# Kernel tuning notes

Measured on AMD Instinct MI355X. Metric: run time of the kernel, lower is better.

Reference implementation:

```python
import jax, jax.numpy as jnp
import numpy as np

TEMPERATURE = 0.1
N, D = 4096, 1024


def setup_inputs() -> dict:
    key = jax.random.key(0)
    k1, k2 = jax.random.split(key)
    return {
        "embeddings1": jax.random.normal(k1, (N, D), dtype=jnp.float32),
        "embeddings2": jax.random.normal(k2, (N, D), dtype=jnp.float32),
    }


def reference(embeddings1, embeddings2):
    # L2-normalize rows (eps matches torch F.normalize default 1e-12)
    e1 = embeddings1 / jnp.maximum(jnp.linalg.norm(embeddings1, axis=1, keepdims=True), 1e-12)
    e2 = embeddings2 / jnp.maximum(jnp.linalg.norm(embeddings2, axis=1, keepdims=True), 1e-12)

    # [N, N] pairwise logits; one GEMM replaces the N^2 Python-loop dots
    logits = jnp.einsum("nd,md->nm", e1, e2) / TEMPERATURE
    expS = jnp.exp(logits)
    diag = jnp.diagonal(expS)

    # denominators EXCLUDE the diagonal term (as in the original loop slicing)
    row_denom = jnp.sum(expS, axis=1) - diag  # sum over j != i of exp(s_ij)
    col_denom = jnp.sum(expS, axis=0) - diag  # sum over i != j of exp(s_ij)

    log_diag = jnp.diagonal(logits)
    sim_12 = jnp.sum(log_diag - jnp.log(row_denom))
    sim_21 = jnp.sum(log_diag - jnp.log(col_denom))
    return (-sim_12, -sim_21)
```

## Files before the change

### kernel.cpp

```cpp
#include <hip/hip_runtime.h>
#include <hip/hip_bf16.h>
#include <stdint.h>

#define NN 4096
#define DD 1024
#define INV_T 10.0f

typedef float f32x4 __attribute__((ext_vector_type(4)));
typedef __bf16 bf16x8 __attribute__((ext_vector_type(8)));

__device__ __forceinline__ unsigned short f2bf(float x) {
  return __builtin_bit_cast(unsigned short, __float2bfloat16(x));
}

__device__ __forceinline__ void gload_lds16(const void* g, void* l) {
  __builtin_amdgcn_global_load_lds(
      (const __attribute__((address_space(1))) void*)g,
      (__attribute__((address_space(3))) void*)l, 16, 0, 0);
}

__global__ __launch_bounds__(256) void nrm_kernel(
    const float* __restrict__ e1, const float* __restrict__ e2,
    unsigned short* __restrict__ e1n, unsigned short* __restrict__ e2n,
    float* __restrict__ log_diag, float* __restrict__ exp_diag,
    float* __restrict__ row_sum, float* __restrict__ col_sum)
{
  const int row  = blockIdx.x;
  const int tid  = threadIdx.x;
  const int lane = tid & 63;
  const int wave = tid >> 6;
  const int64_t base = (int64_t)row * DD;

  const float4 v1 = *reinterpret_cast<const float4*>(e1 + base + tid * 4);
  const float4 v2 = *reinterpret_cast<const float4*>(e2 + base + tid * 4);

  float ss1 = v1.x*v1.x + v1.y*v1.y + v1.z*v1.z + v1.w*v1.w;
  float ss2 = v2.x*v2.x + v2.y*v2.y + v2.z*v2.z + v2.w*v2.w;
  float d12 = v1.x*v2.x + v1.y*v2.y + v1.z*v2.z + v1.w*v2.w;

  #pragma unroll
  for (int off = 1; off < 64; off <<= 1) {
    ss1 += __shfl_xor(ss1, off);
    ss2 += __shfl_xor(ss2, off);
    d12 += __shfl_xor(d12, off);
  }

  __shared__ float red[3][4];
  if (lane == 0) { red[0][wave] = ss1; red[1][wave] = ss2; red[2][wave] = d12; }
  __syncthreads();
  ss1 = red[0][0] + red[0][1] + red[0][2] + red[0][3];
  ss2 = red[1][0] + red[1][1] + red[1][2] + red[1][3];
  d12 = red[2][0] + red[2][1] + red[2][2] + red[2][3];

  const float inv1 = 1.0f / fmaxf(sqrtf(ss1), 1e-12f);
  const float inv2 = 1.0f / fmaxf(sqrtf(ss2), 1e-12f);

  if (tid == 0) {
    const float ld = d12 * inv1 * inv2 * INV_T;
    log_diag[row] = ld;
    exp_diag[row] = __expf(ld);
    row_sum[row] = 0.0f;
    col_sum[row] = 0.0f;
  }

  ushort4 o1, o2;
  o1.x = f2bf(v1.x * inv1); o1.y = f2bf(v1.y * inv1);
  o1.z = f2bf(v1.z * inv1); o1.w = f2bf(v1.w * inv1);
  o2.x = f2bf(v2.x * inv2); o2.y = f2bf(v2.y * inv2);
  o2.z = f2bf(v2.z * inv2); o2.w = f2bf(v2.w * inv2);
  *reinterpret_cast<ushort4*>(e1n + base + tid * 4) = o1;
  *reinterpret_cast<ushort4*>(e2n + base + tid * 4) = o2;
}

__device__ __forceinline__ void stage_khalf(
    const unsigned short* __restrict__ src, int row_base, int kcol,
    unsigned short (*dst)[32], int wave, int lane)
{
  const int r0 = wave * 16 + (lane >> 2);
  const int c  = ((lane & 3) ^ ((lane >> 3) & 3)) * 8;
  gload_lds16(src + (int64_t)(row_base + r0) * DD + kcol + c,
              &dst[wave * 16][0]);
  gload_lds16(src + (int64_t)(row_base + 128 + r0) * DD + kcol + c,
              &dst[128 + wave * 16][0]);
}

__global__ __launch_bounds__(512, 2) void gemm_kernel(
    const unsigned short* __restrict__ A,
    const unsigned short* __restrict__ B,
    float* __restrict__ row_sum, float* __restrict__ col_sum)
{
  __shared__ __align__(16) unsigned short lds_a[2][2][256][32];
  __shared__ __align__(16) unsigned short lds_b[2][2][256][32];

  const int tid  = threadIdx.x;
  const int lane = tid & 63;
  const int wave = tid >> 6;
  const int wm = wave >> 2;
  const int wn = wave & 3;

  const int bid = blockIdx.x;
  const int xcd = bid & 7;
  const int k   = bid >> 3;
  const int brow = ((xcd >> 1) * 4 + (k >> 3)) * 256;
  const int bcol = ((xcd & 1) * 8 + (k & 7)) * 256;

  const int fr = lane & 15;
  const int fq = lane >> 4;
  const int rslot = (fq ^ ((fr >> 1) & 3)) * 8;

  f32x4 acc[8][4] = {};

  stage_khalf(A, brow, 0,  lds_a[0][0], wave, lane);
  stage_khalf(B, bcol, 0,  lds_b[0][0], wave, lane);
  stage_khalf(A, brow, 32, lds_a[0][1], wave, lane);
  stage_khalf(B, bcol, 32, lds_b[0][1], wave, lane);

#define PHASE(KK)                                                               \
  {                                                                             \
    if (pf) { stage_khalf(A, brow, kn + (KK)*32, lds_a[n][KK], wave, lane);     \
              stage_khalf(B, bcol, kn + (KK)*32, lds_b[n][KK], wave, lane); }   \
    bf16x8 a0[4], a1[4], bv[4];                                                 \
    _Pragma("unroll")                                                           \
    for (int i = 0; i < 4; ++i)                                                 \
      a0[i] = *reinterpret_cast<const bf16x8*>(                                 \
          &lds_a[c][KK][wm*128 + i*16 + fr][rslot]);                            \
    _Pragma("unroll")                                                           \
    for (int i = 0; i < 4; ++i)                                                 \
      bv[i] = *reinterpret_cast<const bf16x8*>(                                 \
          &lds_b[c][KK][wn*64 + i*16 + fr][rslot]);                             \
    _Pragma("unroll")                                                           \
    for (int i = 0; i < 4; ++i)                                                 \
      a1[i] = *reinterpret_cast<const bf16x8*>(                                 \
          &lds_a[c][KK][wm*128 + 64 + i*16 + fr][rslot]);                       \
    asm volatile("s_waitcnt lgkmcnt(0)" ::: "memory");                          \
    __builtin_amdgcn_sched_barrier(0);                                          \
    __builtin_amdgcn_s_setprio(1);                                              \
    _Pragma("unroll")                                                           \
    for (int i = 0; i < 4; ++i) {                                               \
      _Pragma("unroll")                                                         \
      for (int j = 0; j < 4; ++j)                                               \
        acc[i][j] = __builtin_amdgcn_mfma_f32_16x16x32_bf16(                    \
            a0[i], bv[j], acc[i][j], 0, 0, 0);                                  \
    }                                                                           \
    _Pragma("unroll")                                                           \
    for (int i = 0; i < 4; ++i) {                                               \
      _Pragma("unroll")                                                         \
      for (int j = 0; j < 4; ++j)                                               \
        acc[4 + i][j] = __builtin_amdgcn_mfma_f32_16x16x32_bf16(                \
            a1[i], bv[j], acc[4 + i][j], 0, 0, 0);                              \
    }                                                                           \
    __builtin_amdgcn_s_setprio(0);                                              \
  }

  #pragma unroll 2
  for (int t = 0; t < DD / 64; ++t) {
    const int c = t & 1;
    const int n = c ^ 1;
    const int kn = (t + 1) * 64;
    const bool pf = (t < DD / 64 - 1);

    asm volatile("s_waitcnt vmcnt(4)" ::: "memory");
    __builtin_amdgcn_s_barrier();
    PHASE(0)

    if (pf) { asm volatile("s_waitcnt vmcnt(4)" ::: "memory"); }
    else    { asm volatile("s_waitcnt vmcnt(0)" ::: "memory"); }
    __builtin_amdgcn_s_barrier();
    PHASE(1)
  }
#undef PHASE

  float rowp[8][4];
  float colp[4];
  #pragma unroll
  for (int mi = 0; mi < 8; ++mi)
    #pragma unroll
    for (int j = 0; j < 4; ++j) rowp[mi][j] = 0.0f;
  #pragma unroll
  for (int ni = 0; ni < 4; ++ni) colp[ni] = 0.0f;

  #pragma unroll
  for (int mi = 0; mi < 8; ++mi) {
    #pragma unroll
    for (int ni = 0; ni < 4; ++ni) {
      #pragma unroll
      for (int j = 0; j < 4; ++j) {
        const float v = __expf(acc[mi][ni][j] * INV_T);
        rowp[mi][j] += v;
        colp[ni]    += v;
      }
    }
  }

  #pragma unroll
  for (int mi = 0; mi < 8; ++mi) {
    #pragma unroll
    for (int j = 0; j < 4; ++j) {
      float r = rowp[mi][j];
      r += __shfl_xor(r, 1);
      r += __shfl_xor(r, 2);
      r += __shfl_xor(r, 4);
      r += __shfl_xor(r, 8);
      if (fr == 0) {
        atomicAdd(&row_sum[brow + wm * 128 + mi * 16 + fq * 4 + j], r);
      }
    }
  }
  #pragma unroll
  for (int ni = 0; ni < 4; ++ni) {
    float cc = colp[ni];
    cc += __shfl_xor(cc, 16);
    cc += __shfl_xor(cc, 32);
    if (lane < 16) {
      atomicAdd(&col_sum[bcol + wn * 64 + ni * 16 + fr], cc);
    }
  }
}

__global__ __launch_bounds__(1024) void fin_kernel(
    const float* __restrict__ row_sum, const float* __restrict__ col_sum,
    const float* __restrict__ log_diag, const float* __restrict__ exp_diag,
    float* __restrict__ out)
{
  const int tid  = threadIdx.x;
  const int lane = tid & 63;
  const int wave = tid >> 6;
  const float* sums = (blockIdx.x == 0) ? row_sum : col_sum;
  float a = 0.0f;
  #pragma unroll
  for (int kk = 0; kk < NN / 1024; ++kk) {
    const int i = tid + kk * 1024;
    a += logf(sums[i] - exp_diag[i]) - log_diag[i];
  }
  #pragma unroll
  for (int off = 1; off < 64; off <<= 1) a += __shfl_xor(a, off);
  __shared__ float r0[16];
  if (lane == 0) r0[wave] = a;
  __syncthreads();
  if (tid == 0) {
    float s = 0.0f;
    #pragma unroll
    for (int w = 0; w < 16; ++w) s += r0[w];
    out[blockIdx.x] = s;
  }
}

extern "C" void kernel_launch(void* const* d_in, const int* in_sizes, int n_in,
                              void* d_out, int out_size, void* d_ws, size_t ws_size,
                              hipStream_t stream) {
  const float* e1 = (const float*)d_in[0];
  const float* e2 = (const float*)d_in[1];
  float* out = (float*)d_out;

  char* ws = (char*)d_ws;
  unsigned short* e1n = (unsigned short*)ws;
  unsigned short* e2n = (unsigned short*)(ws + (size_t)NN * DD * 2);
  float* log_diag = (float*)(ws + (size_t)NN * DD * 4);
  float* exp_diag = log_diag + NN;
  float* row_sum  = exp_diag + NN;
  float* col_sum  = row_sum + NN;

  nrm_kernel<<<NN, 256, 0, stream>>>(e1, e2, e1n, e2n, log_diag, exp_diag,
                                     row_sum, col_sum);
  gemm_kernel<<<256, 512, 0, stream>>>(e1n, e2n, row_sum, col_sum);
  fin_kernel<<<2, 1024, 0, stream>>>(row_sum, col_sum, log_diag, exp_diag, out);
}
```

Before: 57.87 us.

## Switch similarity GEMM from bf16 to fp8 MFMA with scaled quantization

The normalize kernel now quantizes the unit-norm rows to fp8 with a scale of 64, and the GEMM uses fp8 16x16x32 MFMA. A compensating scale is folded into the exponent argument. The GEMM tile shrinks to 256x128 with 512 blocks and higher occupancy, and double buffering now waits on vmcnt(0) each tile. This halves operand bytes and uses the faster fp8 matrix path, at the cost of lower precision in the logits, which are then exponentiated at temperature 0.1.

```diff
diff --git a/kernel.cpp b/kernel.cpp
--- a/kernel.cpp
+++ b/kernel.cpp
@@ -4,14 +4,10 @@
 
 #define NN 4096
 #define DD 1024
-#define INV_T 10.0f
+#define SCL (10.0f / 4096.0f)
 
 typedef float f32x4 __attribute__((ext_vector_type(4)));
-typedef __bf16 bf16x8 __attribute__((ext_vector_type(8)));
-
-__device__ __forceinline__ unsigned short f2bf(float x) {
-  return __builtin_bit_cast(unsigned short, __float2bfloat16(x));
-}
+typedef long long i64;
 
 __device__ __forceinline__ void gload_lds16(const void* g, void* l) {
   __builtin_amdgcn_global_load_lds(
@@ -21,7 +17,7 @@
 
 __global__ __launch_bounds__(256) void nrm_kernel(
     const float* __restrict__ e1, const float* __restrict__ e2,
-    unsigned short* __restrict__ e1n, unsigned short* __restrict__ e2n,
+    uint32_t* __restrict__ e1q, uint32_t* __restrict__ e2q,
     float* __restrict__ log_diag, float* __restrict__ exp_diag,
     float* __restrict__ row_sum, float* __restrict__ col_sum)
 {
@@ -56,136 +52,123 @@
   const float inv2 = 1.0f / fmaxf(sqrtf(ss2), 1e-12f);
 
   if (tid == 0) {
-    const float ld = d12 * inv1 * inv2 * INV_T;
+    const float ld = d12 * inv1 * inv2 * 10.0f;
     log_diag[row] = ld;
     exp_diag[row] = __expf(ld);
     row_sum[row] = 0.0f;
     col_sum[row] = 0.0f;
   }
 
-  ushort4 o1, o2;
-  o1.x = f2bf(v1.x * inv1); o1.y = f2bf(v1.y * inv1);
-  o1.z = f2bf(v1.z * inv1); o1.w = f2bf(v1.w * inv1);
-  o2.x = f2bf(v2.x * inv2); o2.y = f2bf(v2.y * inv2);
-  o2.z = f2bf(v2.z * inv2); o2.w = f2bf(v2.w * inv2);
-  *reinterpret_cast<ushort4*>(e1n + base + tid * 4) = o1;
-  *reinterpret_cast<ushort4*>(e2n + base + tid * 4) = o2;
-}
-
-__device__ __forceinline__ void stage_khalf(
-    const unsigned short* __restrict__ src, int row_base, int kcol,
-    unsigned short (*dst)[32], int wave, int lane)
-{
-  const int r0 = wave * 16 + (lane >> 2);
-  const int c  = ((lane & 3) ^ ((lane >> 3) & 3)) * 8;
-  gload_lds16(src + (int64_t)(row_base + r0) * DD + kcol + c,
-              &dst[wave * 16][0]);
-  gload_lds16(src + (int64_t)(row_base + 128 + r0) * DD + kcol + c,
-              &dst[128 + wave * 16][0]);
-}
-
-__global__ __launch_bounds__(512, 2) void gemm_kernel(
-    const unsigned short* __restrict__ A,
-    const unsigned short* __restrict__ B,
+  const float s1 = inv1 * 64.0f;
+  const float s2 = inv2 * 64.0f;
+  int u1 = __builtin_amdgcn_cvt_pk_fp8_f32(v1.x * s1, v1.y * s1, 0, false);
+  u1     = __builtin_amdgcn_cvt_pk_fp8_f32(v1.z * s1, v1.w * s1, u1, true);
+  int u2 = __builtin_amdgcn_cvt_pk_fp8_f32(v2.x * s2, v2.y * s2, 0, false);
+  u2     = __builtin_amdgcn_cvt_pk_fp8_f32(v2.z * s2, v2.w * s2, u2, true);
+  e1q[row * (DD / 4) + tid] = (uint32_t)u1;
+  e2q[row * (DD / 4) + tid] = (uint32_t)u2;
+}
+
+__global__ __launch_bounds__(512, 4) void gemm_kernel(
+    const uint8_t* __restrict__ A,
+    const uint8_t* __restrict__ B,
     float* __restrict__ row_sum, float* __restrict__ col_sum)
 {
-  __shared__ __align__(16) unsigned short lds_a[2][2][256][32];
-  __shared__ __align__(16) unsigned short lds_b[2][2][256][32];
+  __shared__ __align__(16) uint8_t lds_a[2][256][64];
+  __shared__ __align__(16) uint8_t lds_b[2][128][64];
 
   const int tid  = threadIdx.x;
   const int lane = tid & 63;
   const int wave = tid >> 6;
-  const int wm = wave >> 2;
-  const int wn = wave & 3;
+  const int wm = wave >> 1;
+  const int wn = wave & 1;
 
   const int bid = blockIdx.x;
   const int xcd = bid & 7;
   const int k   = bid >> 3;
-  const int brow = ((xcd >> 1) * 4 + (k >> 3)) * 256;
-  const int bcol = ((xcd & 1) * 8 + (k & 7)) * 256;
+  const int brow = ((xcd >> 1) * 4 + (k >> 4)) * 256;
+  const int bcol = ((xcd & 1) * 16 + (k & 15)) * 128;
 
   const int fr = lane & 15;
   const int fq = lane >> 4;
-  const int rslot = (fq ^ ((fr >> 1) & 3)) * 8;
-
-  f32x4 acc[8][4] = {};
-
-  stage_khalf(A, brow, 0,  lds_a[0][0], wave, lane);
-  stage_khalf(B, bcol, 0,  lds_b[0][0], wave, lane);
-  stage_khalf(A, brow, 32, lds_a[0][1], wave, lane);
-  stage_khalf(B, bcol, 32, lds_b[0][1], wave, lane);
-
-#define PHASE(KK)                                                               \
-  {                                                                             \
-    if (pf) { stage_khalf(A, brow, kn + (KK)*32, lds_a[n][KK], wave, lane);     \
-              stage_khalf(B, bcol, kn + (KK)*32, lds_b[n][KK], wave, lane); }   \
-    bf16x8 a0[4], a1[4], bv[4];                                                 \
-    _Pragma("unroll")                                                           \
-    for (int i = 0; i < 4; ++i)                                                 \
-      a0[i] = *reinterpret_cast<const bf16x8*>(                                 \
-          &lds_a[c][KK][wm*128 + i*16 + fr][rslot]);                            \
-    _Pragma("unroll")                                                           \
-    for (int i = 0; i < 4; ++i)                                                 \
-      bv[i] = *reinterpret_cast<const bf16x8*>(                                 \
-          &lds_b[c][KK][wn*64 + i*16 + fr][rslot]);                             \
-    _Pragma("unroll")                                                           \
-    for (int i = 0; i < 4; ++i)                                                 \
-      a1[i] = *reinterpret_cast<const bf16x8*>(                                 \
-          &lds_a[c][KK][wm*128 + 64 + i*16 + fr][rslot]);                       \
-    asm volatile("s_waitcnt lgkmcnt(0)" ::: "memory");                          \
-    __builtin_amdgcn_sched_barrier(0);                                          \
-    __builtin_amdgcn_s_setprio(1);                                              \
-    _Pragma("unroll")                                                           \
-    for (int i = 0; i < 4; ++i) {                                               \
-      _Pragma("unroll")                                                         \
-      for (int j = 0; j < 4; ++j)                                               \
-        acc[i][j] = __builtin_amdgcn_mfma_f32_16x16x32_bf16(                    \
-            a0[i], bv[j], acc[i][j], 0, 0, 0);                                  \
-    }                                                                           \
-    _Pragma("unroll")                                                           \
-    for (int i = 0; i < 4; ++i) {                                               \
-      _Pragma("unroll")                                                         \
-      for (int j = 0; j < 4; ++j)                                               \
-        acc[4 + i][j] = __builtin_amdgcn_mfma_f32_16x16x32_bf16(                \
-            a1[i], bv[j], acc[4 + i][j], 0, 0, 0);                              \
-    }                                                                           \
-    __builtin_amdgcn_s_setprio(0);                                              \
-  }
+  const int y  = ((fr >> 1) & 3) << 1;
+  const int o0 = ((fq ^ y) * 8);
+
+  const int s_chunk = ((lane & 3) ^ ((lane >> 3) & 3)) * 16;
+  const uint8_t* a_src0 = A + (int64_t)(brow + wave * 32 + (lane >> 2)) * DD + s_chunk;
+  const uint8_t* a_src1 = a_src0 + 16 * DD;
+  const uint8_t* b_src  = B + (int64_t)(bcol + wave * 16 + (lane >> 2)) * DD + s_chunk;
+
+  f32x4 acc[4][4] = {};
+
+#define STAGE(n, kc)                                          \
+  gload_lds16(a_src0 + (kc), &lds_a[n][wave * 32][0]);        \
+  gload_lds16(a_src1 + (kc), &lds_a[n][wave * 32 + 16][0]);   \
+  gload_lds16(b_src  + (kc), &lds_b[n][wave * 16][0]);
+
+#define TILE(c, PF, KC)                                                        \
+  {                                                                            \
+    asm volatile("s_waitcnt vmcnt(0)" ::: "memory");                           \
+    __builtin_amdgcn_s_barrier();                                              \
+    i64 a0[4], b0[4], a1[4], b1[4];                                            \
+    _Pragma("unroll")                                                          \
+    for (int i = 0; i < 4; ++i)                                                \
+      a0[i] = *reinterpret_cast<const i64*>(&lds_a[c][wm*64 + i*16 + fr][o0]); \
+    _Pragma("unroll")                                                          \
+    for (int j = 0; j < 4; ++j)                                                \
+      b0[j] = *reinterpret_cast<const i64*>(&lds_b[c][wn*64 + j*16 + fr][o0]); \
+    _Pragma("unroll")                                                          \
+    for (int i = 0; i < 4; ++i)                                                \
+      a1[i] = *reinterpret_cast<const i64*>(                                   \
+          &lds_a[c][wm*64 + i*16 + fr][o0 ^ 32]);                              \
+    _Pragma("unroll")                                                          \
+    for (int j = 0; j < 4; ++j)                                                \
+      b1[j] = *reinterpret_cast<const i64*>(                                   \
+          &lds_b[c][wn*64 + j*16 + fr][o0 ^ 32]);                              \
+    if (PF) { STAGE((c) ^ 1, KC) }                                             \
+    __builtin_amdgcn_s_setprio(1);                                             \
+    _Pragma("unroll")                                                          \
+    for (int i = 0; i < 4; ++i) {                                              \
+      _Pragma("unroll")                                                        \
+      for (int j = 0; j < 4; ++j)                                              \
+        acc[i][j] = __builtin_amdgcn_mfma_f32_16x16x32_fp8_fp8(                \
+            a0[i], b0[j], acc[i][j], 0, 0, 0);                                 \
+    }                                                                          \
+    _Pragma("unroll")                                                          \
+    for (int i = 0; i < 4; ++i) {                                              \
+      _Pragma("unroll")                                                        \
+      for (int j = 0; j < 4; ++j)                                              \
+        acc[i][j] = __builtin_amdgcn_mfma_f32_16x16x32_fp8_fp8(                \
+            a1[i], b1[j], acc[i][j], 0, 0, 0);                                 \
+    }                                                                          \
+    __builtin_amdgcn_s_setprio(0);                                             \
+  }
+
+  STAGE(0, 0)
 
   #pragma unroll 2
   for (int t = 0; t < DD / 64; ++t) {
-    const int c = t & 1;
-    const int n = c ^ 1;
-    const int kn = (t + 1) * 64;
-    const bool pf = (t < DD / 64 - 1);
-
-    asm volatile("s_waitcnt vmcnt(4)" ::: "memory");
-    __builtin_amdgcn_s_barrier();
-    PHASE(0)
-
-    if (pf) { asm volatile("s_waitcnt vmcnt(4)" ::: "memory"); }
-    else    { asm volatile("s_waitcnt vmcnt(0)" ::: "memory"); }
-    __builtin_amdgcn_s_barrier();
-    PHASE(1)
-  }
-#undef PHASE
-
-  float rowp[8][4];
+    TILE(t & 1, t < DD / 64 - 1, (t + 1) * 64)
+  }
+#undef TILE
+#undef STAGE
+
+  float rowp[4][4];
   float colp[4];
   #pragma unroll
-  for (int mi = 0; mi < 8; ++mi)
+  for (int mi = 0; mi < 4; ++mi)
     #pragma unroll
     for (int j = 0; j < 4; ++j) rowp[mi][j] = 0.0f;
   #pragma unroll
   for (int ni = 0; ni < 4; ++ni) colp[ni] = 0.0f;
 
   #pragma unroll
-  for (int mi = 0; mi < 8; ++mi) {
+  for (int mi = 0; mi < 4; ++mi) {
     #pragma unroll
     for (int ni = 0; ni < 4; ++ni) {
       #pragma unroll
       for (int j = 0; j < 4; ++j) {
-        const float v = __expf(acc[mi][ni][j] * INV_T);
+        const float v = __expf(acc[mi][ni][j] * SCL);
         rowp[mi][j] += v;
         colp[ni]    += v;
       }
@@ -193,7 +176,7 @@
   }
 
   #pragma unroll
-  for (int mi = 0; mi < 8; ++mi) {
+  for (int mi = 0; mi < 4; ++mi) {
     #pragma unroll
     for (int j = 0; j < 4; ++j) {
       float r = rowp[mi][j];
@@ -202,7 +185,7 @@
       r += __shfl_xor(r, 4);
       r += __shfl_xor(r, 8);
       if (fr == 0) {
-        atomicAdd(&row_sum[brow + wm * 128 + mi * 16 + fq * 4 + j], r);
+        atomicAdd(&row_sum[brow + wm * 64 + mi * 16 + fq * 4 + j], r);
       }
     }
   }
@@ -253,15 +236,16 @@
   float* out = (float*)d_out;
 
   char* ws = (char*)d_ws;
-  unsigned short* e1n = (unsigned short*)ws;
-  unsigned short* e2n = (unsigned short*)(ws + (size_t)NN * DD * 2);
-  float* log_diag = (float*)(ws + (size_t)NN * DD * 4);
+  uint32_t* e1q = (uint32_t*)ws;
+  uint32_t* e2q = (uint32_t*)(ws + (size_t)NN * DD);
+  float* log_diag = (float*)(ws + (size_t)NN * DD * 2);
   float* exp_diag = log_diag + NN;
   float* row_sum  = exp_diag + NN;
   float* col_sum  = row_sum + NN;
 
-  nrm_kernel<<<NN, 256, 0, stream>>>(e1, e2, e1n, e2n, log_diag, exp_diag,
+  nrm_kernel<<<NN, 256, 0, stream>>>(e1, e2, e1q, e2q, log_diag, exp_diag,
                                      row_sum, col_sum);
-  gemm_kernel<<<256, 512, 0, stream>>>(e1n, e2n, row_sum, col_sum);
+  gemm_kernel<<<512, 512, 0, stream>>>((const uint8_t*)e1q, (const uint8_t*)e2q,
+                                       row_sum, col_sum);
   fin_kernel<<<2, 1024, 0, stream>>>(row_sum, col_sum, log_diag, exp_diag, out);
 }
```

After: 50.05 us. -13.5%, faster.
